# Performance work log

Measured on AMD Instinct MI355X. Metric: run time of the kernel, lower is better.

The kernel has to match this reference:

```python
import jax, jax.numpy as jnp
import numpy as np

D, H, DFF, MD = 1024, 16, 4096, 128
B, TS, TT = 8, 512, 512
EPS = 1e-6


def _ln(x, s, b):
    m = jnp.mean(x, axis=-1, keepdims=True)
    v = jnp.mean((x - m) ** 2, axis=-1, keepdims=True)
    return (x - m) * jax.lax.rsqrt(v + EPS) * s + b


def _rel_bias(emb, qlen, klen):
    # T5-style bidirectional bucket: [H, qlen, klen]
    q = jnp.arange(qlen)[:, None]
    k = jnp.arange(klen)[None, :]
    rp = k - q
    bucket = jnp.where(rp < 0, jnp.minimum(-rp, MD - 1), jnp.minimum(rp, MD - 1) + MD)
    return emb[bucket].transpose(2, 0, 1)


def _mha(xq, xkv, w_in, b_in, w_out, b_out, bias):
    # nn.MultiheadAttention math: packed in_proj [3D,D], additive attn bias [H,Tq,Tk]
    Bq, Tq, _ = xq.shape
    Tk = xkv.shape[1]
    hd = D // H
    wq, wk, wv = jnp.split(w_in, 3, axis=0)
    bq, bk, bv = jnp.split(b_in, 3, axis=0)
    q = (xq @ wq.T + bq).reshape(Bq, Tq, H, hd).transpose(0, 2, 1, 3)
    k = (xkv @ wk.T + bk).reshape(Bq, Tk, H, hd).transpose(0, 2, 1, 3)
    v = (xkv @ wv.T + bv).reshape(Bq, Tk, H, hd).transpose(0, 2, 1, 3)
    scores = jnp.einsum('bhqd,bhkd->bhqk', q, k) / jnp.sqrt(jnp.asarray(hd, xq.dtype))
    scores = scores + bias[None]
    attn = jax.nn.softmax(scores, axis=-1)
    out = jnp.einsum('bhqk,bhkd->bhqd', attn, v)
    out = out.transpose(0, 2, 1, 3).reshape(Bq, Tq, D)
    return out @ w_out.T + b_out


def setup_inputs() -> dict:
    key = jax.random.key(0)
    ks = jax.random.split(key, 40)
    std = 0.02

    def n(i, shape):
        return jax.random.normal(ks[i], shape, dtype=jnp.float32) * std

    return {
        'src': jax.random.normal(ks[0], (B, TS, D), dtype=jnp.float32),
        'tgt': jax.random.normal(ks[1], (B, TT, D), dtype=jnp.float32),
        # encoder layer
        'enc_in_w': n(2, (3 * D, D)), 'enc_in_b': jnp.zeros((3 * D,)),
        'enc_out_w': n(3, (D, D)), 'enc_out_b': jnp.zeros((D,)),
        'enc_ff1_w': n(4, (DFF, D)), 'enc_ff1_b': jnp.zeros((DFF,)),
        'enc_ff2_w': n(5, (D, DFF)), 'enc_ff2_b': jnp.zeros((D,)),
        'enc_n1_s': jnp.ones((D,)), 'enc_n1_b': jnp.zeros((D,)),
        'enc_n2_s': jnp.ones((D,)), 'enc_n2_b': jnp.zeros((D,)),
        'enc_rel': n(6, (2 * MD, H)),
        # decoder layer
        'dec_sa_in_w': n(7, (3 * D, D)), 'dec_sa_in_b': jnp.zeros((3 * D,)),
        'dec_sa_out_w': n(8, (D, D)), 'dec_sa_out_b': jnp.zeros((D,)),
        'dec_ca_in_w': n(9, (3 * D, D)), 'dec_ca_in_b': jnp.zeros((3 * D,)),
        'dec_ca_out_w': n(10, (D, D)), 'dec_ca_out_b': jnp.zeros((D,)),
        'dec_ff1_w': n(11, (DFF, D)), 'dec_ff1_b': jnp.zeros((DFF,)),
        'dec_ff2_w': n(12, (D, DFF)), 'dec_ff2_b': jnp.zeros((D,)),
        'dec_n1_s': jnp.ones((D,)), 'dec_n1_b': jnp.zeros((D,)),
        'dec_n2_s': jnp.ones((D,)), 'dec_n2_b': jnp.zeros((D,)),
        'dec_n3_s': jnp.ones((D,)), 'dec_n3_b': jnp.zeros((D,)),
        'dec_rel_self': n(13, (2 * MD, H)),
        'dec_rel_cross': n(14, (2 * MD, H)),
    }


def reference(src, tgt,
              enc_in_w, enc_in_b, enc_out_w, enc_out_b,
              enc_ff1_w, enc_ff1_b, enc_ff2_w, enc_ff2_b,
              enc_n1_s, enc_n1_b, enc_n2_s, enc_n2_b, enc_rel,
              dec_sa_in_w, dec_sa_in_b, dec_sa_out_w, dec_sa_out_b,
              dec_ca_in_w, dec_ca_in_b, dec_ca_out_w, dec_ca_out_b,
              dec_ff1_w, dec_ff1_b, dec_ff2_w, dec_ff2_b,
              dec_n1_s, dec_n1_b, dec_n2_s, dec_n2_b, dec_n3_s, dec_n3_b,
              dec_rel_self, dec_rel_cross):
    Ts, Tt = src.shape[1], tgt.shape[1]

    # ---- encoder layer (pre-LN) ----
    eb = _rel_bias(enc_rel, Ts, Ts)  # [H,Ts,Ts]
    x = src
    x = x + _mha(_ln(x, enc_n1_s, enc_n1_b), _ln(x, enc_n1_s, enc_n1_b),
                 enc_in_w, enc_in_b, enc_out_w, enc_out_b, eb)
    h = _ln(x, enc_n2_s, enc_n2_b)
    x = x + (jax.nn.relu(h @ enc_ff1_w.T + enc_ff1_b) @ enc_ff2_w.T + enc_ff2_b)
    memory = x

    # ---- decoder layer (pre-LN) ----
    causal = jnp.where(jnp.arange(Tt)[None, :] > jnp.arange(Tt)[:, None], -jnp.inf, 0.0)
    sb = _rel_bias(dec_rel_self, Tt, Tt) + causal[None]  # [H,Tt,Tt]
    cb = _rel_bias(dec_rel_cross, Tt, Ts)                # [H,Tt,Ts]
    y = tgt
    yn = _ln(y, dec_n1_s, dec_n1_b)
    y = y + _mha(yn, yn, dec_sa_in_w, dec_sa_in_b, dec_sa_out_w, dec_sa_out_b, sb)
    y = y + _mha(_ln(y, dec_n2_s, dec_n2_b), memory,
                 dec_ca_in_w, dec_ca_in_b, dec_ca_out_w, dec_ca_out_b, cb)
    h = _ln(y, dec_n3_s, dec_n3_b)
    y = y + (jax.nn.relu(h @ dec_ff1_w.T + dec_ff1_b) @ dec_ff2_w.T + dec_ff2_b)
    return y
```

## Files before the change

### kernel.cpp

```cpp
#include <hip/hip_runtime.h>

using u16 = unsigned short;

typedef float f32x4 __attribute__((ext_vector_type(4)));
typedef __bf16 bf16x8v __attribute__((ext_vector_type(8)));
typedef bf16x8v bf16x8 __attribute__((may_alias));
typedef u16 u16x8v __attribute__((ext_vector_type(8)));
typedef u16x8v u16x8 __attribute__((may_alias));
typedef u16 u16x4v __attribute__((ext_vector_type(4)));
typedef u16x4v u16x4 __attribute__((may_alias));
typedef float f32x4v __attribute__((ext_vector_type(4)));
typedef f32x4v float4a __attribute__((may_alias));

#define GPTR(p) ((__attribute__((address_space(1))) void*)(p))
#define LPTR(p) ((__attribute__((address_space(3))) void*)(p))

__device__ __forceinline__ u16 f2bf(float f) {
  unsigned u = __builtin_bit_cast(unsigned, f);
  u += 0x7FFFu + ((u >> 16) & 1u);
  return (u16)(u >> 16);
}

__device__ __forceinline__ f32x4 mfma16(bf16x8 a, bf16x8 b, f32x4 c) {
  return __builtin_amdgcn_mfma_f32_16x16x32_bf16(a, b, c, 0, 0, 0);
}

__global__ __launch_bounds__(256) void cvt_bf16(const float* __restrict__ in,
                                                u16* __restrict__ out, int n4) {
  int i = blockIdx.x * 256 + threadIdx.x;
  if (i < n4) {
    float4a v = ((const float4a*)in)[i];
    u16x4 o;
    o[0] = f2bf(v[0]); o[1] = f2bf(v[1]); o[2] = f2bf(v[2]); o[3] = f2bf(v[3]);
    ((u16x4*)out)[i] = o;
  }
}

__global__ __launch_bounds__(256) void ln_k(const float* __restrict__ x,
                                            const float* __restrict__ sc,
                                            const float* __restrict__ bi,
                                            u16* __restrict__ out) {
  const int row = blockIdx.x, tid = threadIdx.x;
  float4a v = ((const float4a*)(x + (size_t)row * 1024))[tid];
  float s1 = v[0] + v[1] + v[2] + v[3];
  float s2 = v[0]*v[0] + v[1]*v[1] + v[2]*v[2] + v[3]*v[3];
#pragma unroll
  for (int off = 32; off; off >>= 1) { s1 += __shfl_xor(s1, off); s2 += __shfl_xor(s2, off); }
  __shared__ float red[8];
  if ((tid & 63) == 0) { red[tid >> 6] = s1; red[4 + (tid >> 6)] = s2; }
  __syncthreads();
  s1 = red[0] + red[1] + red[2] + red[3];
  s2 = red[4] + red[5] + red[6] + red[7];
  const float mean = s1 * (1.f / 1024.f);
  const float rstd = rsqrtf(s2 * (1.f / 1024.f) - mean * mean + 1e-6f);
  float4a s4 = ((const float4a*)sc)[tid];
  float4a b4 = ((const float4a*)bi)[tid];
  u16x4 o;
#pragma unroll
  for (int j = 0; j < 4; j++) o[j] = f2bf((v[j] - mean) * rstd * s4[j] + b4[j]);
  ((u16x4*)(out + (size_t)row * 1024))[tid] = o;
}

template <int BN_T, int MW, int EPI>
__global__ __launch_bounds__(256) void gemm_bt(
    const u16* __restrict__ A, int lda,
    const u16* __restrict__ W, int ldw,
    const float* __restrict__ bias,
    const float* __restrict__ C0, int ldc0,
    void* __restrict__ outv, int ldo, int K) {
  constexpr int BM = 128, BK = 64;
  constexpr int NW = 4 / MW;
  constexpr int FM = BM / MW / 16;
  constexpr int FN = BN_T / NW / 16;
  constexpr int RA = (BM * BK * 2) / 4096;
  constexpr int RB = (BN_T * BK * 2) / 4096;
  __shared__ alignas(16) u16 As[BM * BK];
  __shared__ alignas(16) u16 Bs[BN_T * BK];
  const int tid = threadIdx.x, lane = tid & 63, wv = tid >> 6;
  const int bm = blockIdx.y * BM, bn = blockIdx.x * BN_T;
  const int wr = (wv / NW) * (BM / MW);
  const int wc = (wv % NW) * (BN_T / NW);
  const int la = lane & 15, lk = (lane >> 4) * 8;
  const int srow = wv * 8 + (lane >> 3), scol = (lane & 7) * 8;
  const u16* gA = A + (size_t)(bm + srow) * lda + scol;
  const u16* gB = W + (size_t)(bn + srow) * ldw + scol;
  u16* lA = As + (wv * 8) * BK;
  u16* lB = Bs + (wv * 8) * BK;

  f32x4 acc[FM][FN] = {};

  for (int k0 = 0; k0 < K; k0 += BK) {
    __syncthreads();
#pragma unroll
    for (int r = 0; r < RA; r++)
      __builtin_amdgcn_global_load_lds(GPTR(gA + (size_t)r * 32 * lda + k0),
                                       LPTR(lA + r * 32 * BK), 16, 0, 0);
#pragma unroll
    for (int r = 0; r < RB; r++)
      __builtin_amdgcn_global_load_lds(GPTR(gB + (size_t)r * 32 * ldw + k0),
                                       LPTR(lB + r * 32 * BK), 16, 0, 0);
    __syncthreads();
#pragma unroll
    for (int kk = 0; kk < BK; kk += 32) {
      bf16x8 af[FM], bfr[FN];
#pragma unroll
      for (int m = 0; m < FM; m++) af[m] = *(const bf16x8*)&As[(wr + m * 16 + la) * BK + kk + lk];
#pragma unroll
      for (int n = 0; n < FN; n++) bfr[n] = *(const bf16x8*)&Bs[(wc + n * 16 + la) * BK + kk + lk];
#pragma unroll
      for (int m = 0; m < FM; m++)
#pragma unroll
        for (int n = 0; n < FN; n++)
          acc[m][n] = mfma16(af[m], bfr[n], acc[m][n]);
    }
  }
  float bv[FN];
#pragma unroll
  for (int n = 0; n < FN; n++) bv[n] = bias[bn + wc + n * 16 + la];
#pragma unroll
  for (int m = 0; m < FM; m++) {
#pragma unroll
    for (int j = 0; j < 4; j++) {
      const int row = bm + wr + m * 16 + (lane >> 4) * 4 + j;
#pragma unroll
      for (int n = 0; n < FN; n++) {
        const int col = bn + wc + n * 16 + la;
        float v = acc[m][n][j] + bv[n];
        if constexpr (EPI == 1) v = fmaxf(v, 0.f);
        if constexpr (EPI == 2) {
          ((float*)outv)[(size_t)row * ldo + col] = v + C0[(size_t)row * ldc0 + col];
        } else {
          ((u16*)outv)[(size_t)row * ldo + col] = f2bf(v);
        }
      }
    }
  }
}

template <bool CAUSAL>
__global__ __launch_bounds__(256) void attn_k(
    const u16* __restrict__ Qb, int ldq,
    const u16* __restrict__ Kb, int ldk,
    const u16* __restrict__ Vb, int ldv,
    const float* __restrict__ rel,
    u16* __restrict__ Ob, int ldo,
    int Tq, int Tk) {
  __shared__ alignas(16) u16 Ks[128][72];
  __shared__ alignas(16) u16 Vt[64][136];
  __shared__ alignas(16) u16 Ps[4][16][136];
  __shared__ float biasl[256];
  const int tid = threadIdx.x, lane = tid & 63, w = tid >> 6;
  const int b = blockIdx.y >> 4, h = blockIdx.y & 15;
  const int q0 = blockIdx.x * 64;
  const int la = lane & 15, lg = lane >> 4;

  biasl[tid] = rel[tid * 16 + h];

  const int qr0 = q0 + w * 16;
  const u16* qp = Qb + (size_t)(b * Tq + qr0 + la) * ldq + h * 64 + lg * 8;
  const bf16x8 qf0 = *(const bf16x8*)qp;
  const bf16x8 qf1 = *(const bf16x8*)(qp + 32);

  float m[4], sm[4];
  f32x4 acc[4] = {};
#pragma unroll
  for (int j = 0; j < 4; j++) { m[j] = -1e30f; sm[j] = 0.f; }

  const int kv_end = CAUSAL ? (q0 + 64) : Tk;
  const int srow = tid >> 3, scol = (tid & 7) * 8;
  for (int kv0 = 0; kv0 < kv_end; kv0 += 128) {
    __syncthreads();
#pragma unroll
    for (int r = 0; r < 4; r++) {
      const int row = r * 32 + srow;
      const size_t gr = (size_t)(b * Tk + kv0 + row);
      *(u16x8*)&Ks[row][scol] = *(const u16x8*)&Kb[gr * ldk + h * 64 + scol];
      u16x8 vv = *(const u16x8*)&Vb[gr * ldv + h * 64 + scol];
#pragma unroll
      for (int j = 0; j < 8; j++) Vt[scol + j][row] = vv[j];
    }
    __syncthreads();

    f32x4 s[8];
#pragma unroll
    for (int kvt = 0; kvt < 8; kvt++) {
      const bf16x8 kf0 = *(const bf16x8*)&Ks[kvt * 16 + la][lg * 8];
      const bf16x8 kf1 = *(const bf16x8*)&Ks[kvt * 16 + la][32 + lg * 8];
      f32x4 t = {};
      t = mfma16(qf0, kf0, t);
      t = mfma16(qf1, kf1, t);
      const int kc = kv0 + kvt * 16 + la;
#pragma unroll
      for (int j = 0; j < 4; j++) {
        const int qr = qr0 + lg * 4 + j;
        const int rp = kc - qr;
        const int bucket = rp < 0 ? (rp > -127 ? -rp : 127) : (rp < 127 ? rp : 127) + 128;
        float sv = t[j] * 0.125f + biasl[bucket];
        if (CAUSAL && kc > qr) sv = -1e30f;
        s[kvt][j] = sv;
      }
    }
    float alpha[4];
#pragma unroll
    for (int j = 0; j < 4; j++) {
      float tm = s[0][j];
#pragma unroll
      for (int kvt = 1; kvt < 8; kvt++) tm = fmaxf(tm, s[kvt][j]);
#pragma unroll
      for (int off = 1; off < 16; off <<= 1) tm = fmaxf(tm, __shfl_xor(tm, off));
      const float mn = fmaxf(m[j], tm);
      alpha[j] = __expf(m[j] - mn);
      m[j] = mn;
      float r = 0.f;
#pragma unroll
      for (int kvt = 0; kvt < 8; kvt++) {
        const float p = __expf(s[kvt][j] - mn);
        s[kvt][j] = p;
        r += p;
      }
#pragma unroll
      for (int off = 1; off < 16; off <<= 1) r += __shfl_xor(r, off);
      sm[j] = sm[j] * alpha[j] + r;
    }
#pragma unroll
    for (int kvt = 0; kvt < 8; kvt++)
#pragma unroll
      for (int j = 0; j < 4; j++)
        Ps[w][lg * 4 + j][kvt * 16 + la] = f2bf(s[kvt][j]);
#pragma unroll
    for (int n = 0; n < 4; n++)
#pragma unroll
      for (int j = 0; j < 4; j++)
        acc[n][j] *= alpha[j];
#pragma unroll
    for (int kq = 0; kq < 4; kq++) {
      const bf16x8 pf = *(const bf16x8*)&Ps[w][la][kq * 32 + lg * 8];
#pragma unroll
      for (int n = 0; n < 4; n++) {
        const bf16x8 vf = *(const bf16x8*)&Vt[n * 16 + la][kq * 32 + lg * 8];
        acc[n] = mfma16(pf, vf, acc[n]);
      }
    }
  }
#pragma unroll
  for (int n = 0; n < 4; n++)
#pragma unroll
    for (int j = 0; j < 4; j++) {
      const int qr = qr0 + lg * 4 + j;
      Ob[(size_t)(b * Tq + qr) * ldo + h * 64 + n * 16 + la] = f2bf(acc[n][j] / sm[j]);
    }
}

extern "C" void kernel_launch(void* const* d_in, const int* in_sizes, int n_in,
                              void* d_out, int out_size, void* d_ws, size_t ws_size,
                              hipStream_t stream) {
  (void)in_sizes; (void)n_in; (void)out_size; (void)ws_size;
  const float* src       = (const float*)d_in[0];
  const float* tgt       = (const float*)d_in[1];
  const float* enc_in_w  = (const float*)d_in[2];
  const float* enc_in_b  = (const float*)d_in[3];
  const float* enc_out_w = (const float*)d_in[4];
  const float* enc_out_b = (const float*)d_in[5];
  const float* enc_ff1_w = (const float*)d_in[6];
  const float* enc_ff1_b = (const float*)d_in[7];
  const float* enc_ff2_w = (const float*)d_in[8];
  const float* enc_ff2_b = (const float*)d_in[9];
  const float* enc_n1_s  = (const float*)d_in[10];
  const float* enc_n1_b  = (const float*)d_in[11];
  const float* enc_n2_s  = (const float*)d_in[12];
  const float* enc_n2_b  = (const float*)d_in[13];
  const float* enc_rel   = (const float*)d_in[14];
  const float* dsa_in_w  = (const float*)d_in[15];
  const float* dsa_in_b  = (const float*)d_in[16];
  const float* dsa_out_w = (const float*)d_in[17];
  const float* dsa_out_b = (const float*)d_in[18];
  const float* dca_in_w  = (const float*)d_in[19];
  const float* dca_in_b  = (const float*)d_in[20];
  const float* dca_out_w = (const float*)d_in[21];
  const float* dca_out_b = (const float*)d_in[22];
  const float* dff1_w    = (const float*)d_in[23];
  const float* dff1_b    = (const float*)d_in[24];
  const float* dff2_w    = (const float*)d_in[25];
  const float* dff2_b    = (const float*)d_in[26];
  const float* dn1_s     = (const float*)d_in[27];
  const float* dn1_b     = (const float*)d_in[28];
  const float* dn2_s     = (const float*)d_in[29];
  const float* dn2_b     = (const float*)d_in[30];
  const float* dn3_s     = (const float*)d_in[31];
  const float* dn3_b     = (const float*)d_in[32];
  const float* drel_s    = (const float*)d_in[33];
  const float* drel_c    = (const float*)d_in[34];
  float* fo = (float*)d_out;

  char* w8 = (char*)d_ws;
  float* x_ws  = (float*)(w8 + 0);
  u16* ln_buf  = (u16*)(w8 + 16777216);
  u16* qkv     = (u16*)(w8 + 25165824);
  u16* attn_o  = (u16*)(w8 + 50331648);
  u16* ffh     = qkv;
  u16* memb    = (u16*)(w8 + 58720256);
  u16* wb      = (u16*)(w8 + 67108864);

  u16* w_enc_in  = wb;
  u16* w_enc_out = wb + 3145728;
  u16* w_enc_f1  = wb + 4194304;
  u16* w_enc_f2  = wb + 8388608;
  u16* w_dsa_in  = wb + 12582912;
  u16* w_dsa_out = wb + 15728640;
  u16* w_dca_in  = wb + 16777216;
  u16* w_dca_out = wb + 19922944;
  u16* w_dff1    = wb + 20971520;
  u16* w_dff2    = wb + 25165824;

#define CVT(sp, dp, n) cvt_bf16<<<dim3((n) / 1024), 256, 0, stream>>>(sp, dp, (n) / 4)
  CVT(enc_in_w,  w_enc_in,  3145728);
  CVT(enc_out_w, w_enc_out, 1048576);
  CVT(enc_ff1_w, w_enc_f1,  4194304);
  CVT(enc_ff2_w, w_enc_f2,  4194304);
  CVT(dsa_in_w,  w_dsa_in,  3145728);
  CVT(dsa_out_w, w_dsa_out, 1048576);
  CVT(dca_in_w,  w_dca_in,  3145728);
  CVT(dca_out_w, w_dca_out, 1048576);
  CVT(dff1_w,    w_dff1,    4194304);
  CVT(dff2_w,    w_dff2,    4194304);
#undef CVT

  ln_k<<<dim3(4096), 256, 0, stream>>>(src, enc_n1_s, enc_n1_b, ln_buf);
  gemm_bt<128,2,0><<<dim3(24, 32), 256, 0, stream>>>(ln_buf, 1024, w_enc_in, 1024, enc_in_b, nullptr, 0, qkv, 3072, 1024);
  attn_k<false><<<dim3(8, 128), 256, 0, stream>>>(qkv, 3072, qkv + 1024, 3072, qkv + 2048, 3072, enc_rel, attn_o, 1024, 512, 512);
  gemm_bt<64,4,2><<<dim3(16, 32), 256, 0, stream>>>(attn_o, 1024, w_enc_out, 1024, enc_out_b, src, 1024, x_ws, 1024, 1024);
  ln_k<<<dim3(4096), 256, 0, stream>>>(x_ws, enc_n2_s, enc_n2_b, ln_buf);
  gemm_bt<128,2,1><<<dim3(32, 32), 256, 0, stream>>>(ln_buf, 1024, w_enc_f1, 1024, enc_ff1_b, nullptr, 0, ffh, 4096, 1024);
  gemm_bt<64,4,2><<<dim3(16, 32), 256, 0, stream>>>(ffh, 4096, w_enc_f2, 4096, enc_ff2_b, x_ws, 1024, x_ws, 1024, 4096);
  cvt_bf16<<<dim3(4096), 256, 0, stream>>>(x_ws, memb, 1048576);

  ln_k<<<dim3(4096), 256, 0, stream>>>(tgt, dn1_s, dn1_b, ln_buf);
  gemm_bt<128,2,0><<<dim3(24, 32), 256, 0, stream>>>(ln_buf, 1024, w_dsa_in, 1024, dsa_in_b, nullptr, 0, qkv, 3072, 1024);
  attn_k<true><<<dim3(8, 128), 256, 0, stream>>>(qkv, 3072, qkv + 1024, 3072, qkv + 2048, 3072, drel_s, attn_o, 1024, 512, 512);
  gemm_bt<64,4,2><<<dim3(16, 32), 256, 0, stream>>>(attn_o, 1024, w_dsa_out, 1024, dsa_out_b, tgt, 1024, fo, 1024, 1024);

  ln_k<<<dim3(4096), 256, 0, stream>>>(fo, dn2_s, dn2_b, ln_buf);
  gemm_bt<64,4,0><<<dim3(16, 32), 256, 0, stream>>>(ln_buf, 1024, w_dca_in, 1024, dca_in_b, nullptr, 0, qkv, 3072, 1024);
  gemm_bt<128,2,0><<<dim3(16, 32), 256, 0, stream>>>(memb, 1024, w_dca_in + 1048576, 1024, dca_in_b + 1024, nullptr, 0, qkv + 1024, 3072, 1024);
  attn_k<false><<<dim3(8, 128), 256, 0, stream>>>(qkv, 3072, qkv + 1024, 3072, qkv + 2048, 3072, drel_c, attn_o, 1024, 512, 512);
  gemm_bt<64,4,2><<<dim3(16, 32), 256, 0, stream>>>(attn_o, 1024, w_dca_out, 1024, dca_out_b, fo, 1024, fo, 1024, 1024);

  ln_k<<<dim3(4096), 256, 0, stream>>>(fo, dn3_s, dn3_b, ln_buf);
  gemm_bt<128,2,1><<<dim3(32, 32), 256, 0, stream>>>(ln_buf, 1024, w_dff1, 1024, dff1_b, nullptr, 0, ffh, 4096, 1024);
  gemm_bt<64,4,2><<<dim3(16, 32), 256, 0, stream>>>(ffh, 4096, w_dff2, 4096, dff2_b, fo, 1024, fo, 1024, 4096);
}
```

Measured before the change: 703.6 us.

## Add double-buffered GEMM, LDS swizzle, XCD remap, split-K FF2, fused weight conversion

Merges the ten weight-conversion launches into one kernel. The GEMM gains an optional double-buffered LDS prefetch path with manual vmcnt waits, an XOR swizzle on LDS columns to cut bank conflicts, and a block-index remap that groups tiles per XCD. The FF2 GEMMs switch to split-K over two z-slices with wider tiles, and a follow-up elementwise kernel adds the partial sums. This trades extra memory passes and launches for better overlap and occupancy, and the hand-written waitcnt counts are fragile.

```diff
diff --git a/kernel.cpp b/kernel.cpp
--- a/kernel.cpp
+++ b/kernel.cpp
@@ -25,15 +25,41 @@
   return __builtin_amdgcn_mfma_f32_16x16x32_bf16(a, b, c, 0, 0, 0);
 }
 
-__global__ __launch_bounds__(256) void cvt_bf16(const float* __restrict__ in,
-                                                u16* __restrict__ out, int n4) {
-  int i = blockIdx.x * 256 + threadIdx.x;
-  if (i < n4) {
-    float4a v = ((const float4a*)in)[i];
-    u16x4 o;
-    o[0] = f2bf(v[0]); o[1] = f2bf(v[1]); o[2] = f2bf(v[2]); o[3] = f2bf(v[3]);
-    ((u16x4*)out)[i] = o;
-  }
+struct Srcs { const float* s[10]; };
+
+__global__ __launch_bounds__(256) void cvt_all(Srcs srcs, u16* __restrict__ dst) {
+  constexpr int off[11] = {0, 786432, 1048576, 2097152, 3145728,
+                           3932160, 4194304, 4980736, 5242880, 6291456, 7340032};
+  const int i = blockIdx.x * 256 + threadIdx.x;
+  int r = 0;
+#pragma unroll
+  for (int j = 1; j < 10; j++) r += (i >= off[j]);
+  float4a v = ((const float4a*)srcs.s[r])[i - off[r]];
+  u16x4 o;
+  o[0] = f2bf(v[0]); o[1] = f2bf(v[1]); o[2] = f2bf(v[2]); o[3] = f2bf(v[3]);
+  ((u16x4*)dst)[i] = o;
+}
+
+__global__ __launch_bounds__(256) void add_cvt(const float* __restrict__ a,
+                                               const float* __restrict__ b,
+                                               u16* __restrict__ o) {
+  const int i = blockIdx.x * 256 + threadIdx.x;
+  float4a va = ((const float4a*)a)[i];
+  float4a vb = ((const float4a*)b)[i];
+  u16x4 ov;
+#pragma unroll
+  for (int j = 0; j < 4; j++) ov[j] = f2bf(va[j] + vb[j]);
+  ((u16x4*)o)[i] = ov;
+}
+
+__global__ __launch_bounds__(256) void add_f32(float* __restrict__ o,
+                                               const float* __restrict__ b) {
+  const int i = blockIdx.x * 256 + threadIdx.x;
+  float4a vo = ((float4a*)o)[i];
+  float4a vb = ((const float4a*)b)[i];
+#pragma unroll
+  for (int j = 0; j < 4; j++) vo[j] += vb[j];
+  ((float4a*)o)[i] = vo;
 }
 
 __global__ __launch_bounds__(256) void ln_k(const float* __restrict__ x,
@@ -61,62 +87,108 @@
   ((u16x4*)(out + (size_t)row * 1024))[tid] = o;
 }
 
-template <int BN_T, int MW, int EPI>
+template <int BN_T, int MW, int EPI, int PF>
 __global__ __launch_bounds__(256) void gemm_bt(
     const u16* __restrict__ A, int lda,
     const u16* __restrict__ W, int ldw,
     const float* __restrict__ bias,
     const float* __restrict__ C0, int ldc0,
-    void* __restrict__ outv, int ldo, int K) {
+    void* __restrict__ outv, int ldo, int K,
+    float* __restrict__ part) {
   constexpr int BM = 128, BK = 64;
   constexpr int NW = 4 / MW;
   constexpr int FM = BM / MW / 16;
   constexpr int FN = BN_T / NW / 16;
   constexpr int RA = (BM * BK * 2) / 4096;
   constexpr int RB = (BN_T * BK * 2) / 4096;
-  __shared__ alignas(16) u16 As[BM * BK];
-  __shared__ alignas(16) u16 Bs[BN_T * BK];
+  constexpr int NB = PF ? 2 : 1;
+  __shared__ alignas(16) u16 As[NB][BM * BK];
+  __shared__ alignas(16) u16 Bs[NB][BN_T * BK];
   const int tid = threadIdx.x, lane = tid & 63, wv = tid >> 6;
-  const int bm = blockIdx.y * BM, bn = blockIdx.x * BN_T;
+  const int kb = (EPI == 3) ? blockIdx.z * K : 0;
+
+  const int gx = gridDim.x;
+  const int nwg = gx * gridDim.y;
+  const int orig = blockIdx.y * gx + blockIdx.x;
+  const int qq = nwg >> 3, rr = nwg & 7;
+  const int xcd = orig & 7, idx = orig >> 3;
+  const int wg = (xcd < rr ? xcd * (qq + 1) : rr * (qq + 1) + (xcd - rr) * qq) + idx;
+  const int bm = (wg / gx) * BM, bn = (wg % gx) * BN_T;
+
   const int wr = (wv / NW) * (BM / MW);
   const int wc = (wv % NW) * (BN_T / NW);
-  const int la = lane & 15, lk = (lane >> 4) * 8;
-  const int srow = wv * 8 + (lane >> 3), scol = (lane & 7) * 8;
+  const int la = lane & 15, lg = lane >> 4;
+  const int r7 = la & 7;
+  const int srow = wv * 8 + (lane >> 3);
+  const int scol = ((lane & 7) ^ (lane >> 3)) << 3;
   const u16* gA = A + (size_t)(bm + srow) * lda + scol;
   const u16* gB = W + (size_t)(bn + srow) * ldw + scol;
-  u16* lA = As + (wv * 8) * BK;
-  u16* lB = Bs + (wv * 8) * BK;
 
   f32x4 acc[FM][FN] = {};
 
-  for (int k0 = 0; k0 < K; k0 += BK) {
-    __syncthreads();
+  auto stage = [&](int buf, int k0) {
 #pragma unroll
     for (int r = 0; r < RA; r++)
       __builtin_amdgcn_global_load_lds(GPTR(gA + (size_t)r * 32 * lda + k0),
-                                       LPTR(lA + r * 32 * BK), 16, 0, 0);
+                                       LPTR(&As[buf][(wv * 8 + r * 32) * BK]), 16, 0, 0);
 #pragma unroll
     for (int r = 0; r < RB; r++)
       __builtin_amdgcn_global_load_lds(GPTR(gB + (size_t)r * 32 * ldw + k0),
-                                       LPTR(lB + r * 32 * BK), 16, 0, 0);
-    __syncthreads();
+                                       LPTR(&Bs[buf][(wv * 8 + r * 32) * BK]), 16, 0, 0);
+  };
+
+  auto compute = [&](int buf) {
 #pragma unroll
     for (int kk = 0; kk < BK; kk += 32) {
+      const int off = ((((kk >> 3) + lg) ^ r7) << 3);
       bf16x8 af[FM], bfr[FN];
 #pragma unroll
-      for (int m = 0; m < FM; m++) af[m] = *(const bf16x8*)&As[(wr + m * 16 + la) * BK + kk + lk];
-#pragma unroll
-      for (int n = 0; n < FN; n++) bfr[n] = *(const bf16x8*)&Bs[(wc + n * 16 + la) * BK + kk + lk];
+      for (int m = 0; m < FM; m++)
+        af[m] = *(const bf16x8*)&As[buf][(wr + m * 16 + la) * BK + off];
+#pragma unroll
+      for (int n = 0; n < FN; n++)
+        bfr[n] = *(const bf16x8*)&Bs[buf][(wc + n * 16 + la) * BK + off];
 #pragma unroll
       for (int m = 0; m < FM; m++)
 #pragma unroll
         for (int n = 0; n < FN; n++)
           acc[m][n] = mfma16(af[m], bfr[n], acc[m][n]);
     }
+  };
+
+  if constexpr (PF) {
+    stage(0, kb);
+    int buf = 0;
+    const int NT = K / BK;
+    for (int t = 0; t < NT; ++t) {
+      if (t + 1 < NT) {
+        stage(buf ^ 1, kb + (t + 1) * BK);
+        if constexpr (RA + RB == 8)
+          asm volatile("s_waitcnt vmcnt(8)" ::: "memory");
+        else
+          asm volatile("s_waitcnt vmcnt(6)" ::: "memory");
+      } else {
+        asm volatile("s_waitcnt vmcnt(0)" ::: "memory");
+      }
+      __builtin_amdgcn_s_barrier();
+      __builtin_amdgcn_sched_barrier(0);
+      compute(buf);
+      __builtin_amdgcn_s_barrier();
+      buf ^= 1;
+    }
+  } else {
+    for (int k0 = 0; k0 < K; k0 += BK) {
+      __syncthreads();
+      stage(0, kb + k0);
+      __syncthreads();
+      compute(0);
+    }
   }
+
+  const bool addb = (EPI != 3) || (blockIdx.z == 0);
   float bv[FN];
 #pragma unroll
-  for (int n = 0; n < FN; n++) bv[n] = bias[bn + wc + n * 16 + la];
+  for (int n = 0; n < FN; n++) bv[n] = addb ? bias[bn + wc + n * 16 + la] : 0.f;
 #pragma unroll
   for (int m = 0; m < FM; m++) {
 #pragma unroll
@@ -129,6 +201,11 @@
         if constexpr (EPI == 1) v = fmaxf(v, 0.f);
         if constexpr (EPI == 2) {
           ((float*)outv)[(size_t)row * ldo + col] = v + C0[(size_t)row * ldc0 + col];
+        } else if constexpr (EPI == 3) {
+          if (blockIdx.z == 0)
+            ((float*)outv)[(size_t)row * ldo + col] = v + C0[(size_t)row * ldc0 + col];
+          else
+            part[(size_t)row * ldo + col] = v;
         } else {
           ((u16*)outv)[(size_t)row * ldo + col] = f2bf(v);
         }
@@ -312,40 +389,32 @@
   u16* w_dff1    = wb + 20971520;
   u16* w_dff2    = wb + 25165824;
 
-#define CVT(sp, dp, n) cvt_bf16<<<dim3((n) / 1024), 256, 0, stream>>>(sp, dp, (n) / 4)
-  CVT(enc_in_w,  w_enc_in,  3145728);
-  CVT(enc_out_w, w_enc_out, 1048576);
-  CVT(enc_ff1_w, w_enc_f1,  4194304);
-  CVT(enc_ff2_w, w_enc_f2,  4194304);
-  CVT(dsa_in_w,  w_dsa_in,  3145728);
-  CVT(dsa_out_w, w_dsa_out, 1048576);
-  CVT(dca_in_w,  w_dca_in,  3145728);
-  CVT(dca_out_w, w_dca_out, 1048576);
-  CVT(dff1_w,    w_dff1,    4194304);
-  CVT(dff2_w,    w_dff2,    4194304);
-#undef CVT
+  Srcs srcs = {{enc_in_w, enc_out_w, enc_ff1_w, enc_ff2_w, dsa_in_w,
+                dsa_out_w, dca_in_w, dca_out_w, dff1_w, dff2_w}};
+  cvt_all<<<dim3(28672), 256, 0, stream>>>(srcs, wb);
 
   ln_k<<<dim3(4096), 256, 0, stream>>>(src, enc_n1_s, enc_n1_b, ln_buf);
-  gemm_bt<128,2,0><<<dim3(24, 32), 256, 0, stream>>>(ln_buf, 1024, w_enc_in, 1024, enc_in_b, nullptr, 0, qkv, 3072, 1024);
+  gemm_bt<128,2,0,0><<<dim3(24, 32), 256, 0, stream>>>(ln_buf, 1024, w_enc_in, 1024, enc_in_b, nullptr, 0, qkv, 3072, 1024, nullptr);
   attn_k<false><<<dim3(8, 128), 256, 0, stream>>>(qkv, 3072, qkv + 1024, 3072, qkv + 2048, 3072, enc_rel, attn_o, 1024, 512, 512);
-  gemm_bt<64,4,2><<<dim3(16, 32), 256, 0, stream>>>(attn_o, 1024, w_enc_out, 1024, enc_out_b, src, 1024, x_ws, 1024, 1024);
+  gemm_bt<64,4,2,1><<<dim3(16, 32), 256, 0, stream>>>(attn_o, 1024, w_enc_out, 1024, enc_out_b, src, 1024, x_ws, 1024, 1024, nullptr);
   ln_k<<<dim3(4096), 256, 0, stream>>>(x_ws, enc_n2_s, enc_n2_b, ln_buf);
-  gemm_bt<128,2,1><<<dim3(32, 32), 256, 0, stream>>>(ln_buf, 1024, w_enc_f1, 1024, enc_ff1_b, nullptr, 0, ffh, 4096, 1024);
-  gemm_bt<64,4,2><<<dim3(16, 32), 256, 0, stream>>>(ffh, 4096, w_enc_f2, 4096, enc_ff2_b, x_ws, 1024, x_ws, 1024, 4096);
-  cvt_bf16<<<dim3(4096), 256, 0, stream>>>(x_ws, memb, 1048576);
+  gemm_bt<128,2,1,0><<<dim3(32, 32), 256, 0, stream>>>(ln_buf, 1024, w_enc_f1, 1024, enc_ff1_b, nullptr, 0, ffh, 4096, 1024, nullptr);
+  gemm_bt<128,2,3,1><<<dim3(8, 32, 2), 256, 0, stream>>>(ffh, 4096, w_enc_f2, 4096, enc_ff2_b, x_ws, 1024, x_ws, 1024, 2048, fo);
+  add_cvt<<<dim3(4096), 256, 0, stream>>>(x_ws, fo, memb);
 
   ln_k<<<dim3(4096), 256, 0, stream>>>(tgt, dn1_s, dn1_b, ln_buf);
-  gemm_bt<128,2,0><<<dim3(24, 32), 256, 0, stream>>>(ln_buf, 1024, w_dsa_in, 1024, dsa_in_b, nullptr, 0, qkv, 3072, 1024);
+  gemm_bt<128,2,0,0><<<dim3(24, 32), 256, 0, stream>>>(ln_buf, 1024, w_dsa_in, 1024, dsa_in_b, nullptr, 0, qkv, 3072, 1024, nullptr);
   attn_k<true><<<dim3(8, 128), 256, 0, stream>>>(qkv, 3072, qkv + 1024, 3072, qkv + 2048, 3072, drel_s, attn_o, 1024, 512, 512);
-  gemm_bt<64,4,2><<<dim3(16, 32), 256, 0, stream>>>(attn_o, 1024, w_dsa_out, 1024, dsa_out_b, tgt, 1024, fo, 1024, 1024);
+  gemm_bt<64,4,2,1><<<dim3(16, 32), 256, 0, stream>>>(attn_o, 1024, w_dsa_out, 1024, dsa_out_b, tgt, 1024, fo, 1024, 1024, nullptr);
 
   ln_k<<<dim3(4096), 256, 0, stream>>>(fo, dn2_s, dn2_b, ln_buf);
-  gemm_bt<64,4,0><<<dim3(16, 32), 256, 0, stream>>>(ln_buf, 1024, w_dca_in, 1024, dca_in_b, nullptr, 0, qkv, 3072, 1024);
-  gemm_bt<128,2,0><<<dim3(16, 32), 256, 0, stream>>>(memb, 1024, w_dca_in + 1048576, 1024, dca_in_b + 1024, nullptr, 0, qkv + 1024, 3072, 1024);
+  gemm_bt<64,4,0,1><<<dim3(16, 32), 256, 0, stream>>>(ln_buf, 1024, w_dca_in, 1024, dca_in_b, nullptr, 0, qkv, 3072, 1024, nullptr);
+  gemm_bt<128,2,0,0><<<dim3(16, 32), 256, 0, stream>>>(memb, 1024, w_dca_in + 1048576, 1024, dca_in_b + 1024, nullptr, 0, qkv + 1024, 3072, 1024, nullptr);
   attn_k<false><<<dim3(8, 128), 256, 0, stream>>>(qkv, 3072, qkv + 1024, 3072, qkv + 2048, 3072, drel_c, attn_o, 1024, 512, 512);
-  gemm_bt<64,4,2><<<dim3(16, 32), 256, 0, stream>>>(attn_o, 1024, w_dca_out, 1024, dca_out_b, fo, 1024, fo, 1024, 1024);
+  gemm_bt<64,4,2,1><<<dim3(16, 32), 256, 0, stream>>>(attn_o, 1024, w_dca_out, 1024, dca_out_b, fo, 1024, fo, 1024, 1024, nullptr);
 
   ln_k<<<dim3(4096), 256, 0, stream>>>(fo, dn3_s, dn3_b, ln_buf);
-  gemm_bt<128,2,1><<<dim3(32, 32), 256, 0, stream>>>(ln_buf, 1024, w_dff1, 1024, dff1_b, nullptr, 0, ffh, 4096, 1024);
-  gemm_bt<64,4,2><<<dim3(16, 32), 256, 0, stream>>>(ffh, 4096, w_dff2, 4096, dff2_b, fo, 1024, fo, 1024, 4096);
-}
+  gemm_bt<128,2,1,0><<<dim3(32, 32), 256, 0, stream>>>(ln_buf, 1024, w_dff1, 1024, dff1_b, nullptr, 0, ffh, 4096, 1024, nullptr);
+  gemm_bt<128,2,3,1><<<dim3(8, 32, 2), 256, 0, stream>>>(ffh, 4096, w_dff2, 4096, dff2_b, fo, 1024, fo, 1024, 2048, x_ws);
+  add_f32<<<dim3(4096), 256, 0, stream>>>(fo, x_ws);
+}
```

Result: faster. 613.0 us (-12.9%).
